# Optimization experiments

Measured on AMD Instinct MI355X. Metric: run time of the kernel, lower is better.

Reference implementation:

```python
import jax, jax.numpy as jnp
import numpy as np

R = 32          # grid_resolution
C_DIM = 128
HID = 128
N_BLOCKS = 5
PAD = 0.1
N_FREQ = 10

def setup_inputs() -> dict:
    key = jax.random.key(0)
    ks = jax.random.split(key, 10)
    B, T = 4, 65536
    s = 0.05
    return {
        "p": jax.random.uniform(ks[0], (B, T, 3), jnp.float32, -0.5, 0.5),
        "fc_pos_w": jax.random.normal(ks[1], (60, 2 * HID), jnp.float32) * s,
        "fc_pos_b": jax.random.normal(ks[2], (2 * HID,), jnp.float32) * s,
        "fc0_w": jax.random.normal(ks[3], (N_BLOCKS, 2 * HID, HID), jnp.float32) * s,
        "fc0_b": jax.random.normal(ks[4], (N_BLOCKS, HID), jnp.float32) * s,
        "fc1_w": jax.random.normal(ks[5], (N_BLOCKS, HID, HID), jnp.float32) * s,
        "fc1_b": jax.random.normal(ks[6], (N_BLOCKS, HID), jnp.float32) * s,
        "sc_w": jax.random.normal(ks[7], (N_BLOCKS, 2 * HID, HID), jnp.float32) * s,
        "fc_c_w": jax.random.normal(ks[8], (HID, C_DIM), jnp.float32) * s,
        "fc_c_b": jax.random.normal(ks[9], (C_DIM,), jnp.float32) * s,
    }

def _pos_enc(p):
    # NeRF-style: per frequency append sin then cos -> [B,T,3*2*10]=60
    freqs = (2.0 ** jnp.arange(N_FREQ, dtype=p.dtype)) * np.pi
    outs = []
    for i in range(N_FREQ):
        outs.append(jnp.sin(freqs[i] * p))
        outs.append(jnp.cos(freqs[i] * p))
    return jnp.concatenate(outs, axis=-1)

def _grid_index(p):
    # normalize_3d_coordinate + coordinate2index (3d)
    p_nor = p / (1.0 + PAD + 1e-3) + 0.5
    p_nor = jnp.clip(p_nor, 0.0, 1.0 - 1e-3)
    xi = (p_nor * R).astype(jnp.int32)
    return xi[..., 0] + R * (xi[..., 1] + R * xi[..., 2])  # [B,T]

def _resblock(x, w0, b0, w1, b1, ws):
    # ResnetBlockFC: fc_0(relu(x)) -> fc_1(relu(net)); shortcut Linear(no bias)
    net = jnp.maximum(x, 0) @ w0 + b0
    dx = jnp.maximum(net, 0) @ w1 + b1
    return x @ ws + dx

def _seg_max(c, idx):  # c [T,D], idx [T]
    return jax.ops.segment_max(c, idx, num_segments=R ** 3)

def _seg_sum(c, idx):
    return jax.ops.segment_sum(c, idx, num_segments=R ** 3)

def reference(p, fc_pos_w, fc_pos_b, fc0_w, fc0_b, fc1_w, fc1_b, sc_w, fc_c_w, fc_c_b):
    B = p.shape[0]
    index = _grid_index(p)                               # [B,T] int32
    net = _pos_enc(p) @ fc_pos_w + fc_pos_b              # [B,T,256]
    net = _resblock(net, fc0_w[0], fc0_b[0], fc1_w[0], fc1_b[0], sc_w[0])  # [B,T,128]
    for i in range(1, N_BLOCKS):
        # pool_local: scatter_max per voxel, gather back at each point
        fea = jax.vmap(_seg_max)(net, index)             # [B,R^3,128]
        pooled = jnp.take_along_axis(fea, index[..., None], axis=1)  # [B,T,128]
        net = jnp.concatenate([net, pooled], axis=-1)    # [B,T,256]
        net = _resblock(net, fc0_w[i], fc0_b[i], fc1_w[i], fc1_b[i], sc_w[i])
    c = net @ fc_c_w + fc_c_b                            # [B,T,128]
    # generate_grid_features: scatter_mean into R^3 voxels (empty voxels -> 0)
    sums = jax.vmap(_seg_sum)(c, index)                  # [B,R^3,128]
    cnt = jax.vmap(_seg_sum)(jnp.ones(index.shape + (1,), c.dtype), index)
    mean = sums / jnp.maximum(cnt, 1.0)
    fea_grid = mean.transpose(0, 2, 1).reshape(B, C_DIM, R, R, R)
    return fea_grid
```

## Files before the change

### kernel.cpp

```cpp
#include <hip/hip_runtime.h>

typedef _Float16 hf;
typedef _Float16 hf8 __attribute__((ext_vector_type(8)));
typedef float f32x4 __attribute__((ext_vector_type(4)));

static constexpr int BATCH = 4;
static constexpr int TPTS  = 65536;
static constexpr int NPTS  = BATCH * TPTS;
static constexpr int R3    = 32768;
static constexpr int NVOX  = BATCH * R3;

static constexpr int OFF_WPOS = 0;
static constexpr int OFF_W0   = 16384;
static constexpr int OFF_W1   = 180224;
static constexpr int OFF_WSC  = 262144;
static constexpr int OFF_WC   = 425984;
static constexpr int NCHUNKS  = 55296;

__device__ constexpr int kpat(int g, int j) { return (j & 3) + 4 * g + 16 * (j >> 2); }

#define MFMA16(a, b, c) __builtin_amdgcn_mfma_f32_16x16x32_f16((a), (b), (c), 0, 0, 0)

__device__ inline hf8 relu8(hf8 a) {
#pragma unroll
  for (int i = 0; i < 8; ++i) a[i] = (a[i] > (hf)0) ? a[i] : (hf)0;
  return a;
}
__device__ inline f32x4 splat4(float v) {
  f32x4 r; r[0] = v; r[1] = v; r[2] = v; r[3] = v; return r;
}
__device__ inline hf8 ldfrag(const hf* __restrict__ base, int kc, int nt, int NT, int lane) {
  return *(const hf8*)(base + (((size_t)(kc * NT + nt) * 64 + lane) << 3));
}

__global__ __launch_bounds__(256) void k_prep(
    const float* __restrict__ wpos, const float* __restrict__ w0,
    const float* __restrict__ w1,  const float* __restrict__ wsc,
    const float* __restrict__ wc,  hf* __restrict__ fr)
{
  const int cid = blockIdx.x * 256 + threadIdx.x;
  if (cid >= NCHUNKS) return;
  const float* src; hf* dst; int NT, N, kmax, loc;
  if (cid < 2048) {
    src = wpos; dst = fr + OFF_WPOS; NT = 16; N = 256; kmax = 60; loc = cid;
  } else if (cid < 22528) {
    int l5 = cid - 2048; int i = l5 >> 12; loc = l5 & 4095;
    src = w0 + (size_t)i * 32768; dst = fr + OFF_W0 + (size_t)i * 32768;
    NT = 8; N = 128; kmax = 256;
  } else if (cid < 32768) {
    int l5 = cid - 22528; int i = l5 >> 11; loc = l5 & 2047;
    src = w1 + (size_t)i * 16384; dst = fr + OFF_W1 + (size_t)i * 16384;
    NT = 8; N = 128; kmax = 128;
  } else if (cid < 53248) {
    int l5 = cid - 32768; int i = l5 >> 12; loc = l5 & 4095;
    src = wsc + (size_t)i * 32768; dst = fr + OFF_WSC + (size_t)i * 32768;
    NT = 8; N = 128; kmax = 256;
  } else {
    loc = cid - 53248; src = wc; dst = fr + OFF_WC; NT = 8; N = 128; kmax = 128;
  }
  const int lane = loc & 63;
  const int rest = loc >> 6;
  const int nt = rest % NT, kc = rest / NT;
  const int g = lane >> 4;
  const int n = nt * 16 + (lane & 15);
  union { hf8 h; hf f[8]; } o;
#pragma unroll
  for (int j = 0; j < 8; ++j) {
    int k = kc * 32 + kpat(g, j);
    o.f[j] = (k < kmax) ? (hf)src[(size_t)k * N + n] : (hf)0;
  }
  *(hf8*)(dst + ((size_t)loc << 3)) = o.h;
}

__global__ __launch_bounds__(256) void k_idxcnt(
    const float* __restrict__ p, int* __restrict__ idxbuf, int* __restrict__ cnt)
{
  const int t = blockIdx.x * 256 + threadIdx.x;
  const float px = p[(size_t)t * 3 + 0];
  const float py = p[(size_t)t * 3 + 1];
  const float pz = p[(size_t)t * 3 + 2];
  float nx = fminf(fmaxf(px / 1.101f + 0.5f, 0.0f), 0.999f);
  float ny = fminf(fmaxf(py / 1.101f + 0.5f, 0.0f), 0.999f);
  float nz = fminf(fmaxf(pz / 1.101f + 0.5f, 0.0f), 0.999f);
  const int iv = (int)(nx * 32.f) + 32 * (int)(ny * 32.f) + 1024 * (int)(nz * 32.f);
  idxbuf[t] = iv;
  atomicAdd(&cnt[((t >> 16) << 15) | iv], 1);
}

__global__ __launch_bounds__(256) void k_scan(
    const int* __restrict__ cnt, int* __restrict__ start, int* __restrict__ total)
{
  __shared__ int s[256];
  __shared__ int base_s;
  const int tid = threadIdx.x;
  const int v0 = blockIdx.x * 512;
  const int a = cnt[v0 + 2 * tid], b = cnt[v0 + 2 * tid + 1];
  const int sum = a + b;
  s[tid] = sum;
  __syncthreads();
  for (int off = 1; off < 256; off <<= 1) {
    int x = (tid >= off) ? s[tid - off] : 0;
    __syncthreads();
    s[tid] += x;
    __syncthreads();
  }
  if (tid == 255) base_s = atomicAdd(total, s[255]);
  __syncthreads();
  const int excl = base_s + s[tid] - sum;
  start[v0 + 2 * tid]     = excl;
  start[v0 + 2 * tid + 1] = excl + a;
}

__global__ __launch_bounds__(256) void k_fill(
    int* __restrict__ idxbuf, int* __restrict__ start, int* __restrict__ svox)
{
  const int t = blockIdx.x * 256 + threadIdx.x;
  const int bv = ((t >> 16) << 15) | idxbuf[t];
  const int pos = atomicAdd(&start[bv], 1);
  svox[pos] = bv;
  idxbuf[t] = pos;
}

__global__ __launch_bounds__(256, 4) void k_fused0(
    const float* __restrict__ p, const hf* __restrict__ fr,
    const float* __restrict__ bpos,
    const hf* __restrict__ w0f, const hf* __restrict__ w1f,
    const hf* __restrict__ wscf,
    const float* __restrict__ b0, const float* __restrict__ b1,
    const int* __restrict__ spos, hf* __restrict__ net)
{
  __shared__ __align__(16) hf swX[16384];
  __shared__ int sp[64];
  const int tid = threadIdx.x;
  const int wv = tid >> 6, lane = tid & 63;
  const int r = lane & 15, g = lane >> 4;
  const int t0 = blockIdx.x * 64;

  if (tid < 64) sp[tid] = spos[t0 + tid];

  if (tid < 64) {
    const int mt = tid >> 4, rr = tid & 15;
    *(unsigned long long*)(swX + (((mt * 2 + 1) * 64 + 48 + rr) << 3) + 4) = 0ull;
  }
#pragma unroll
  for (int i = 0; i < 8; ++i) {
    const int tau = tid + i * 256;
    if (tau >= 1920) break;
    const int pt = (int)(((unsigned)tau * 34953u) >> 20);
    const int a  = tau - pt * 30;
    const int fi = (a * 11) >> 5;
    const int comp = a - 3 * fi;
    const float pc = p[(size_t)(t0 + pt) * 3 + comp];
    const float ang = (float)(1 << fi) * 3.14159274101257324f * pc;
    const float sv = __sinf(ang), cv = __cosf(ang);
    const int mt = pt >> 4, rr = pt & 15;
    const int ks = 6 * fi + comp;
    {
      const int kc = ks >> 5, kk = ks & 31, gg = (kk >> 2) & 3;
      const int e = (kk & 3) + 4 * (kk >> 4);
      swX[(((mt * 2 + kc) * 64 + gg * 16 + rr) << 3) + e] = (hf)sv;
    }
    {
      const int kco = ks + 3;
      const int kc = kco >> 5, kk = kco & 31, gg = (kk >> 2) & 3;
      const int e = (kk & 3) + 4 * (kk >> 4);
      swX[(((mt * 2 + kc) * 64 + gg * 16 + rr) << 3) + e] = (hf)cv;
    }
  }
  __syncthreads();

  f32x4 acc[4][4];
#pragma unroll
  for (int nf = 0; nf < 4; ++nf) {
    float bv = bpos[wv * 64 + nf * 16 + r];
#pragma unroll
    for (int mf = 0; mf < 4; ++mf) acc[mf][nf] = splat4(bv);
  }
#pragma unroll
  for (int kc = 0; kc < 2; ++kc) {
    hf8 a[4];
#pragma unroll
    for (int mf = 0; mf < 4; ++mf)
      a[mf] = *(const hf8*)(swX + (((mf * 2 + kc) * 64 + lane) << 3));
#pragma unroll
    for (int nf = 0; nf < 4; ++nf) {
      hf8 b = ldfrag(fr + OFF_WPOS, kc, wv * 4 + nf, 16, lane);
#pragma unroll
      for (int mf = 0; mf < 4; ++mf) acc[mf][nf] = MFMA16(a[mf], b, acc[mf][nf]);
    }
  }
  __syncthreads();

#pragma unroll
  for (int mf = 0; mf < 4; ++mf)
#pragma unroll
    for (int nf = 0; nf < 4; ++nf)
#pragma unroll
      for (int reg = 0; reg < 4; ++reg) {
        int rr = 4 * g + reg;
        int c  = wv * 64 + nf * 16 + r;
        int kc = c >> 5;
        int kk = c & 31;
        int gg = (kk >> 2) & 3;
        int e  = (kk & 3) + 4 * (kk >> 4);
        int slot = gg * 16 + ((rr + gg) & 15);
        swX[(((size_t)(mf * 8 + kc) * 64 + slot) << 3) + e] = (hf)acc[mf][nf][reg];
      }
  __syncthreads();

  const int wm = wv >> 1, wn = wv & 1;
  const int lidx = g * 16 + ((r + g) & 15);

  f32x4 h[2][4], d[2][4];
#pragma unroll
  for (int nf = 0; nf < 4; ++nf) {
    const int n = wn * 64 + nf * 16 + r;
    const float bh = b0[n], bd = b1[n];
#pragma unroll
    for (int mf = 0; mf < 2; ++mf) { h[mf][nf] = splat4(bh); d[mf][nf] = splat4(bd); }
  }
#pragma unroll 2
  for (int kc = 0; kc < 8; ++kc) {
    hf8 a[2], ar[2];
#pragma unroll
    for (int mf = 0; mf < 2; ++mf) {
      a[mf] = *(const hf8*)(swX + (((size_t)((wm * 2 + mf) * 8 + kc) * 64 + lidx) << 3));
      ar[mf] = relu8(a[mf]);
    }
#pragma unroll
    for (int nf = 0; nf < 4; ++nf) {
      hf8 bw0 = ldfrag(w0f, kc, wn * 4 + nf, 8, lane);
      hf8 bws = ldfrag(wscf, kc, wn * 4 + nf, 8, lane);
#pragma unroll
      for (int mf = 0; mf < 2; ++mf) {
        h[mf][nf] = MFMA16(ar[mf], bw0, h[mf][nf]);
        d[mf][nf] = MFMA16(a[mf],  bws, d[mf][nf]);
      }
    }
  }
  __syncthreads();

#pragma unroll
  for (int mf = 0; mf < 2; ++mf)
#pragma unroll
    for (int nf = 0; nf < 4; ++nf)
#pragma unroll
      for (int reg = 0; reg < 4; ++reg) {
        int m = wm * 32 + mf * 16 + 4 * g + reg;
        int k = wn * 64 + nf * 16 + r;
        float hv = fmaxf(h[mf][nf][reg], 0.f);
        int mt = m >> 4, rr = m & 15;
        int kc = k >> 5, kk = k & 31;
        int gg = (kk >> 2) & 3;
        int e = (kk & 3) + 4 * (kk >> 4);
        int slot = gg * 16 + ((rr + gg) & 15);
        swX[(((size_t)(mt * 4 + kc) * 64 + slot) << 3) + e] = (hf)hv;
      }
  __syncthreads();

#pragma unroll
  for (int kc = 0; kc < 4; ++kc) {
    hf8 a[2];
#pragma unroll
    for (int mf = 0; mf < 2; ++mf)
      a[mf] = *(const hf8*)(swX + (((size_t)((wm * 2 + mf) * 4 + kc) * 64 + lidx) << 3));
#pragma unroll
    for (int nf = 0; nf < 4; ++nf) {
      hf8 bw1 = ldfrag(w1f, kc, wn * 4 + nf, 8, lane);
#pragma unroll
      for (int mf = 0; mf < 2; ++mf) d[mf][nf] = MFMA16(a[mf], bw1, d[mf][nf]);
    }
  }

#pragma unroll
  for (int mf = 0; mf < 2; ++mf)
#pragma unroll
    for (int nf = 0; nf < 4; ++nf)
#pragma unroll
      for (int reg = 0; reg < 4; ++reg) {
        int m = wm * 32 + mf * 16 + 4 * g + reg;
        int n = wn * 64 + nf * 16 + r;
        net[(size_t)sp[m] * 128 + n] = (hf)d[mf][nf][reg];
      }
}

__global__ __launch_bounds__(256) void k_pool(
    const hf* __restrict__ net, const int* __restrict__ start,
    const int* __restrict__ cnt, hf* __restrict__ fea)
{
  const int gid = blockIdx.x * 256 + threadIdx.x;
  const int bv = gid >> 4;
  const int q = gid & 15;
  const int n = cnt[bv];
  if (n == 0) return;
  const int end = start[bv], beg = end - n;
  float m[8];
#pragma unroll
  for (int e = 0; e < 8; ++e) m[e] = -1e30f;
  for (int i = beg; i < end; ++i) {
    union { uint4 u; hf h[8]; } x;
    x.u = *(const uint4*)(net + (size_t)i * 128 + 8 * q);
#pragma unroll
    for (int e = 0; e < 8; ++e) m[e] = fmaxf(m[e], (float)x.h[e]);
  }
  union { uint4 u; hf h[8]; } o;
#pragma unroll
  for (int e = 0; e < 8; ++e) o.h[e] = (hf)m[e];
  *(uint4*)(fea + ((size_t)bv << 7) + 8 * q) = o.u;
}

__global__ __launch_bounds__(256, 2) void k_res(
    hf* __restrict__ net, const hf* __restrict__ fea,
    const int* __restrict__ svox,
    const hf* __restrict__ w0f, const hf* __restrict__ w1f,
    const hf* __restrict__ wscf,
    const float* __restrict__ b0, const float* __restrict__ b1)
{
  __shared__ __align__(16) hf swX[32768];
  const int tid = threadIdx.x;
  const int wv = tid >> 6, lane = tid & 63;
  const int r = lane & 15, g = lane >> 4;
  const int wm = wv >> 1, wn = wv & 1;
  const int t0 = blockIdx.x * 128;
  const int lidx = g * 16 + ((r + g) & 15);

  for (int cc = tid; cc < 4096; cc += 256) {
    const int cl = cc & 63;
    const int kc = (cc >> 6) & 7;
    const int mt = cc >> 9;
    const int rr = cl & 15, gg = cl >> 4;
    const int t = t0 + mt * 16 + rr;
    const int c1 = kc * 32 + 4 * gg;
    union { hf8 h; uint2 u2[2]; } x;
    const hf* srcp;
    if (kc < 4) {
      srcp = net + (size_t)t * 128 + c1;
    } else {
      srcp = fea + (((size_t)svox[t]) << 7) + (c1 - 128);
    }
    x.u2[0] = *(const uint2*)(srcp);
    x.u2[1] = *(const uint2*)(srcp + 16);
    const int slot = gg * 16 + ((rr + gg) & 15);
    *(hf8*)(swX + (((size_t)((cc & ~63) + slot)) << 3)) = x.h;
  }
  __syncthreads();

  f32x4 h[4][4], d[4][4];
#pragma unroll
  for (int nf = 0; nf < 4; ++nf) {
    const int n = wn * 64 + nf * 16 + r;
    const float bh = b0[n], bd = b1[n];
#pragma unroll
    for (int mf = 0; mf < 4; ++mf) { h[mf][nf] = splat4(bh); d[mf][nf] = splat4(bd); }
  }
#pragma unroll 2
  for (int kc = 0; kc < 8; ++kc) {
    hf8 a[4], ar[4];
#pragma unroll
    for (int mf = 0; mf < 4; ++mf) {
      a[mf] = *(const hf8*)(swX + (((size_t)((wm * 4 + mf) * 8 + kc) * 64 + lidx) << 3));
      ar[mf] = relu8(a[mf]);
    }
#pragma unroll
    for (int nf = 0; nf < 4; ++nf) {
      hf8 bw0 = ldfrag(w0f, kc, wn * 4 + nf, 8, lane);
      hf8 bws = ldfrag(wscf, kc, wn * 4 + nf, 8, lane);
#pragma unroll
      for (int mf = 0; mf < 4; ++mf) {
        h[mf][nf] = MFMA16(ar[mf], bw0, h[mf][nf]);
        d[mf][nf] = MFMA16(a[mf],  bws, d[mf][nf]);
      }
    }
  }
  __syncthreads();

#pragma unroll
  for (int mf = 0; mf < 4; ++mf)
#pragma unroll
    for (int nf = 0; nf < 4; ++nf)
#pragma unroll
      for (int reg = 0; reg < 4; ++reg) {
        int m = wm * 64 + mf * 16 + 4 * g + reg;
        int k = wn * 64 + nf * 16 + r;
        float hv = fmaxf(h[mf][nf][reg], 0.f);
        int mt = m >> 4, rr = m & 15;
        int kc = k >> 5, kk = k & 31;
        int gg = (kk >> 2) & 3;
        int e = (kk & 3) + 4 * (kk >> 4);
        int slot = gg * 16 + ((rr + gg) & 15);
        swX[(((size_t)(mt * 4 + kc) * 64 + slot) << 3) + e] = (hf)hv;
      }
  __syncthreads();

#pragma unroll
  for (int kc = 0; kc < 4; ++kc) {
    hf8 a[4];
#pragma unroll
    for (int mf = 0; mf < 4; ++mf)
      a[mf] = *(const hf8*)(swX + (((size_t)((wm * 4 + mf) * 4 + kc) * 64 + lidx) << 3));
#pragma unroll
    for (int nf = 0; nf < 4; ++nf) {
      hf8 bw1 = ldfrag(w1f, kc, wn * 4 + nf, 8, lane);
#pragma unroll
      for (int mf = 0; mf < 4; ++mf) d[mf][nf] = MFMA16(a[mf], bw1, d[mf][nf]);
    }
  }

#pragma unroll
  for (int mf = 0; mf < 4; ++mf)
#pragma unroll
    for (int nf = 0; nf < 4; ++nf)
#pragma unroll
      for (int reg = 0; reg < 4; ++reg) {
        int m = wm * 64 + mf * 16 + 4 * g + reg;
        int n = wn * 64 + nf * 16 + r;
        net[(size_t)(t0 + m) * 128 + n] = (hf)d[mf][nf][reg];
      }
}

__global__ __launch_bounds__(256, 4) void k_fcc(
    hf* __restrict__ net, const hf* __restrict__ wcf, const float* __restrict__ bc)
{
  __shared__ __align__(16) hf swX[16384];
  const int tid = threadIdx.x;
  const int wv = tid >> 6, lane = tid & 63;
  const int r = lane & 15, g = lane >> 4;
  const int wm = wv >> 1, wn = wv & 1;
  const int t0 = blockIdx.x * 128;

  for (int cc = tid; cc < 2048; cc += 256) {
    const int cl = cc & 63;
    const int kc = (cc >> 6) & 3;
    const int mt = cc >> 8;
    const int rr = cl & 15, gg = cl >> 4;
    const int t = t0 + mt * 16 + rr;
    const int c1 = kc * 32 + 4 * gg;
    union { hf8 h; uint2 u2[2]; } x;
    const hf* srcp = net + (size_t)t * 128 + c1;
    x.u2[0] = *(const uint2*)(srcp);
    x.u2[1] = *(const uint2*)(srcp + 16);
    *(hf8*)(swX + ((size_t)cc << 3)) = x.h;
  }
  __syncthreads();

  f32x4 d[4][4];
#pragma unroll
  for (int nf = 0; nf < 4; ++nf) {
    float bv = bc[wn * 64 + nf * 16 + r];
#pragma unroll
    for (int mf = 0; mf < 4; ++mf) d[mf][nf] = splat4(bv);
  }
#pragma unroll
  for (int kc = 0; kc < 4; ++kc) {
    hf8 a[4];
#pragma unroll
    for (int mf = 0; mf < 4; ++mf)
      a[mf] = *(const hf8*)(swX + (((size_t)((wm * 4 + mf) * 4 + kc) * 64 + lane) << 3));
#pragma unroll
    for (int nf = 0; nf < 4; ++nf) {
      hf8 b = ldfrag(wcf, kc, wn * 4 + nf, 8, lane);
#pragma unroll
      for (int mf = 0; mf < 4; ++mf) d[mf][nf] = MFMA16(a[mf], b, d[mf][nf]);
    }
  }

#pragma unroll
  for (int mf = 0; mf < 4; ++mf)
#pragma unroll
    for (int nf = 0; nf < 4; ++nf)
#pragma unroll
      for (int reg = 0; reg < 4; ++reg) {
        int m = wm * 64 + mf * 16 + 4 * g + reg;
        int n = wn * 64 + nf * 16 + r;
        net[(size_t)(t0 + m) * 128 + n] = (hf)d[mf][nf][reg];
      }
}

__global__ __launch_bounds__(256) void k_write(
    const hf* __restrict__ cbuf, const int* __restrict__ start,
    const int* __restrict__ cnt, float* __restrict__ out)
{
  __shared__ float tile[128 * 65];
  const int tid = threadIdx.x;
  const int grp = tid >> 4, q = tid & 15;
  const int g0 = blockIdx.x * 64;
  for (int vl = grp; vl < 64; vl += 16) {
    const int bv = g0 + vl;
    const int n = cnt[bv];
    const int end = start[bv], beg = end - n;
    float s[8] = {0, 0, 0, 0, 0, 0, 0, 0};
    for (int i = beg; i < end; ++i) {
      union { uint4 u; hf h[8]; } x;
      x.u = *(const uint4*)(cbuf + (size_t)i * 128 + 8 * q);
#pragma unroll
      for (int e = 0; e < 8; ++e) s[e] += (float)x.h[e];
    }
    const float inv = 1.0f / fmaxf((float)n, 1.0f);
#pragma unroll
    for (int e = 0; e < 8; ++e) tile[(8 * q + e) * 65 + vl] = s[e] * inv;
  }
  __syncthreads();
  const int b = g0 >> 15, v0 = g0 & 32767;
  for (int i = tid; i < 8192; i += 256) {
    const int c = i >> 6, vl = i & 63;
    out[(((size_t)(b * 128 + c)) << 15) + v0 + vl] = tile[c * 65 + vl];
  }
}

extern "C" void kernel_launch(void* const* d_in, const int* in_sizes, int n_in,
                              void* d_out, int out_size, void* d_ws, size_t ws_size,
                              hipStream_t stream)
{
  const float* p    = (const float*)d_in[0];
  const float* wpos = (const float*)d_in[1];
  const float* bpos = (const float*)d_in[2];
  const float* w0   = (const float*)d_in[3];
  const float* b0   = (const float*)d_in[4];
  const float* w1   = (const float*)d_in[5];
  const float* b1   = (const float*)d_in[6];
  const float* wsc  = (const float*)d_in[7];
  const float* wc   = (const float*)d_in[8];
  const float* bc   = (const float*)d_in[9];

  char* ws = (char*)d_ws;
  int* idxbuf = (int*)ws;
  hf*  net    = (hf*)(ws + (1u << 20));
  hf*  fea    = (hf*)(ws + (65u << 20));
  int* cnt32  = (int*)(ws + (97u << 20));
  int* total  = (int*)(ws + (97u << 20) + 0x80000);
  int* startb = (int*)(ws + (97u << 20) + 0x80400);
  int* svox   = (int*)(ws + (97u << 20) + 0x100400);
  hf*  fr     = (hf*)d_out;

  k_prep<<<216, 256, 0, stream>>>(wpos, w0, w1, wsc, wc, fr);

  hipMemsetAsync(cnt32, 0, 0x80000 + 0x400, stream);
  k_idxcnt<<<NPTS / 256, 256, 0, stream>>>(p, idxbuf, cnt32);
  k_scan<<<NVOX / 512, 256, 0, stream>>>(cnt32, startb, total);
  k_fill<<<NPTS / 256, 256, 0, stream>>>(idxbuf, startb, svox);

  k_fused0<<<NPTS / 64, 256, 0, stream>>>(p, fr, bpos,
      fr + OFF_W0, fr + OFF_W1, fr + OFF_WSC, b0, b1, idxbuf, net);

  for (int i = 1; i < 5; ++i) {
    k_pool<<<(NVOX * 16) / 256, 256, 0, stream>>>(net, startb, cnt32, fea);
    k_res<<<NPTS / 128, 256, 0, stream>>>(net, fea, svox,
        fr + OFF_W0 + (size_t)i * 32768, fr + OFF_W1 + (size_t)i * 16384,
        fr + OFF_WSC + (size_t)i * 32768, b0 + i * 128, b1 + i * 128);
  }

  k_fcc<<<NPTS / 128, 256, 0, stream>>>(net, fr + OFF_WC, bc);
  k_write<<<NVOX / 64, 256, 0, stream>>>(net, startb, cnt32, (float*)d_out);
}
```

Measured before the change: 636.1 us.

## Fuse final fc_c projection into last resblock and pool by sorted point runs

The final fc_c GEMM is folded into the last k_res launch. The block output is staged back into LDS in the swizzled A-fragment layout and multiplied by the fc_c weights, so one global write and read of net is avoided. k_pool now walks sorted points (svox) in runs of equal voxel id instead of launching 16 threads per voxel, including empty ones. This removes the idle threads for empty voxels, but load balance now depends on run length, and a run that crosses a group boundary is scanned entirely by the group where it starts.

```diff
diff --git a/kernel.cpp b/kernel.cpp
--- a/kernel.cpp
+++ b/kernel.cpp
@@ -285,36 +285,44 @@
 }
 
 __global__ __launch_bounds__(256) void k_pool(
-    const hf* __restrict__ net, const int* __restrict__ start,
-    const int* __restrict__ cnt, hf* __restrict__ fea)
-{
-  const int gid = blockIdx.x * 256 + threadIdx.x;
-  const int bv = gid >> 4;
-  const int q = gid & 15;
-  const int n = cnt[bv];
-  if (n == 0) return;
-  const int end = start[bv], beg = end - n;
-  float m[8];
-#pragma unroll
-  for (int e = 0; e < 8; ++e) m[e] = -1e30f;
-  for (int i = beg; i < end; ++i) {
-    union { uint4 u; hf h[8]; } x;
-    x.u = *(const uint4*)(net + (size_t)i * 128 + 8 * q);
-#pragma unroll
-    for (int e = 0; e < 8; ++e) m[e] = fmaxf(m[e], (float)x.h[e]);
-  }
-  union { uint4 u; hf h[8]; } o;
-#pragma unroll
-  for (int e = 0; e < 8; ++e) o.h[e] = (hf)m[e];
-  *(uint4*)(fea + ((size_t)bv << 7) + 8 * q) = o.u;
-}
-
+    const hf* __restrict__ net, const int* __restrict__ svox,
+    hf* __restrict__ fea)
+{
+  const int tid = threadIdx.x;
+  const int grp = tid >> 4, q = tid & 15;
+  const int gbeg = blockIdx.x * 128 + grp * 8;
+  const int gend = gbeg + 8;
+  int i = gbeg;
+  while (i < gend) {
+    const int v = svox[i];
+    if (i != 0 && svox[i - 1] == v) { ++i; continue; }
+    float m[8];
+#pragma unroll
+    for (int e = 0; e < 8; ++e) m[e] = -1e30f;
+    int j = i;
+    do {
+      union { uint4 u; hf h[8]; } x;
+      x.u = *(const uint4*)(net + (size_t)j * 128 + 8 * q);
+#pragma unroll
+      for (int e = 0; e < 8; ++e) m[e] = fmaxf(m[e], (float)x.h[e]);
+      ++j;
+    } while (j < NPTS && svox[j] == v);
+    union { uint4 u; hf h[8]; } o;
+#pragma unroll
+    for (int e = 0; e < 8; ++e) o.h[e] = (hf)m[e];
+    *(uint4*)(fea + ((size_t)v << 7) + 8 * q) = o.u;
+    i = j;
+  }
+}
+
+template <int LAST>
 __global__ __launch_bounds__(256, 2) void k_res(
     hf* __restrict__ net, const hf* __restrict__ fea,
     const int* __restrict__ svox,
     const hf* __restrict__ w0f, const hf* __restrict__ w1f,
     const hf* __restrict__ wscf,
-    const float* __restrict__ b0, const float* __restrict__ b1)
+    const float* __restrict__ b0, const float* __restrict__ b1,
+    const hf* __restrict__ wcf, const float* __restrict__ bc)
 {
   __shared__ __align__(16) hf swX[32768];
   const int tid = threadIdx.x;
@@ -406,74 +414,67 @@
     }
   }
 
-#pragma unroll
-  for (int mf = 0; mf < 4; ++mf)
-#pragma unroll
-    for (int nf = 0; nf < 4; ++nf)
-#pragma unroll
-      for (int reg = 0; reg < 4; ++reg) {
-        int m = wm * 64 + mf * 16 + 4 * g + reg;
-        int n = wn * 64 + nf * 16 + r;
-        net[(size_t)(t0 + m) * 128 + n] = (hf)d[mf][nf][reg];
-      }
-}
-
-__global__ __launch_bounds__(256, 4) void k_fcc(
-    hf* __restrict__ net, const hf* __restrict__ wcf, const float* __restrict__ bc)
-{
-  __shared__ __align__(16) hf swX[16384];
-  const int tid = threadIdx.x;
-  const int wv = tid >> 6, lane = tid & 63;
-  const int r = lane & 15, g = lane >> 4;
-  const int wm = wv >> 1, wn = wv & 1;
-  const int t0 = blockIdx.x * 128;
-
-  for (int cc = tid; cc < 2048; cc += 256) {
-    const int cl = cc & 63;
-    const int kc = (cc >> 6) & 3;
-    const int mt = cc >> 8;
-    const int rr = cl & 15, gg = cl >> 4;
-    const int t = t0 + mt * 16 + rr;
-    const int c1 = kc * 32 + 4 * gg;
-    union { hf8 h; uint2 u2[2]; } x;
-    const hf* srcp = net + (size_t)t * 128 + c1;
-    x.u2[0] = *(const uint2*)(srcp);
-    x.u2[1] = *(const uint2*)(srcp + 16);
-    *(hf8*)(swX + ((size_t)cc << 3)) = x.h;
-  }
-  __syncthreads();
-
-  f32x4 d[4][4];
-#pragma unroll
-  for (int nf = 0; nf < 4; ++nf) {
-    float bv = bc[wn * 64 + nf * 16 + r];
-#pragma unroll
-    for (int mf = 0; mf < 4; ++mf) d[mf][nf] = splat4(bv);
-  }
-#pragma unroll
-  for (int kc = 0; kc < 4; ++kc) {
-    hf8 a[4];
+  if (LAST) {
+    __syncthreads();
 #pragma unroll
     for (int mf = 0; mf < 4; ++mf)
-      a[mf] = *(const hf8*)(swX + (((size_t)((wm * 4 + mf) * 4 + kc) * 64 + lane) << 3));
+#pragma unroll
+      for (int nf = 0; nf < 4; ++nf)
+#pragma unroll
+        for (int reg = 0; reg < 4; ++reg) {
+          int m = wm * 64 + mf * 16 + 4 * g + reg;
+          int k = wn * 64 + nf * 16 + r;
+          int mt = m >> 4, rr = m & 15;
+          int kc = k >> 5, kk = k & 31;
+          int gg = (kk >> 2) & 3;
+          int e = (kk & 3) + 4 * (kk >> 4);
+          int slot = gg * 16 + ((rr + gg) & 15);
+          swX[(((size_t)(mt * 4 + kc) * 64 + slot) << 3) + e] = (hf)d[mf][nf][reg];
+        }
+    __syncthreads();
+
+    f32x4 c2[4][4];
 #pragma unroll
     for (int nf = 0; nf < 4; ++nf) {
-      hf8 b = ldfrag(wcf, kc, wn * 4 + nf, 8, lane);
-#pragma unroll
-      for (int mf = 0; mf < 4; ++mf) d[mf][nf] = MFMA16(a[mf], b, d[mf][nf]);
-    }
-  }
-
-#pragma unroll
-  for (int mf = 0; mf < 4; ++mf)
-#pragma unroll
-    for (int nf = 0; nf < 4; ++nf)
-#pragma unroll
-      for (int reg = 0; reg < 4; ++reg) {
-        int m = wm * 64 + mf * 16 + 4 * g + reg;
-        int n = wn * 64 + nf * 16 + r;
-        net[(size_t)(t0 + m) * 128 + n] = (hf)d[mf][nf][reg];
-      }
+      float bv = bc[wn * 64 + nf * 16 + r];
+#pragma unroll
+      for (int mf = 0; mf < 4; ++mf) c2[mf][nf] = splat4(bv);
+    }
+#pragma unroll
+    for (int kc = 0; kc < 4; ++kc) {
+      hf8 a[4];
+#pragma unroll
+      for (int mf = 0; mf < 4; ++mf)
+        a[mf] = *(const hf8*)(swX + (((size_t)((wm * 4 + mf) * 4 + kc) * 64 + lidx) << 3));
+#pragma unroll
+      for (int nf = 0; nf < 4; ++nf) {
+        hf8 bw = ldfrag(wcf, kc, wn * 4 + nf, 8, lane);
+#pragma unroll
+        for (int mf = 0; mf < 4; ++mf) c2[mf][nf] = MFMA16(a[mf], bw, c2[mf][nf]);
+      }
+    }
+#pragma unroll
+    for (int mf = 0; mf < 4; ++mf)
+#pragma unroll
+      for (int nf = 0; nf < 4; ++nf)
+#pragma unroll
+        for (int reg = 0; reg < 4; ++reg) {
+          int m = wm * 64 + mf * 16 + 4 * g + reg;
+          int n = wn * 64 + nf * 16 + r;
+          net[(size_t)(t0 + m) * 128 + n] = (hf)c2[mf][nf][reg];
+        }
+  } else {
+#pragma unroll
+    for (int mf = 0; mf < 4; ++mf)
+#pragma unroll
+      for (int nf = 0; nf < 4; ++nf)
+#pragma unroll
+        for (int reg = 0; reg < 4; ++reg) {
+          int m = wm * 64 + mf * 16 + 4 * g + reg;
+          int n = wn * 64 + nf * 16 + r;
+          net[(size_t)(t0 + m) * 128 + n] = (hf)d[mf][nf][reg];
+        }
+  }
 }
 
 __global__ __launch_bounds__(256) void k_write(
@@ -542,13 +543,18 @@
   k_fused0<<<NPTS / 64, 256, 0, stream>>>(p, fr, bpos,
       fr + OFF_W0, fr + OFF_W1, fr + OFF_WSC, b0, b1, idxbuf, net);
 
-  for (int i = 1; i < 5; ++i) {
-    k_pool<<<(NVOX * 16) / 256, 256, 0, stream>>>(net, startb, cnt32, fea);
-    k_res<<<NPTS / 128, 256, 0, stream>>>(net, fea, svox,
+  for (int i = 1; i < 4; ++i) {
+    k_pool<<<NPTS / 128, 256, 0, stream>>>(net, svox, fea);
+    k_res<0><<<NPTS / 128, 256, 0, stream>>>(net, fea, svox,
         fr + OFF_W0 + (size_t)i * 32768, fr + OFF_W1 + (size_t)i * 16384,
-        fr + OFF_WSC + (size_t)i * 32768, b0 + i * 128, b1 + i * 128);
-  }
-
-  k_fcc<<<NPTS / 128, 256, 0, stream>>>(net, fr + OFF_WC, bc);
+        fr + OFF_WSC + (size_t)i * 32768, b0 + i * 128, b1 + i * 128,
+        nullptr, nullptr);
+  }
+  k_pool<<<NPTS / 128, 256, 0, stream>>>(net, svox, fea);
+  k_res<1><<<NPTS / 128, 256, 0, stream>>>(net, fea, svox,
+      fr + OFF_W0 + (size_t)4 * 32768, fr + OFF_W1 + (size_t)4 * 16384,
+      fr + OFF_WSC + (size_t)4 * 32768, b0 + 4 * 128, b1 + 4 * 128,
+      fr + OFF_WC, bc);
+
   k_write<<<NVOX / 64, 256, 0, stream>>>(net, startb, cnt32, (float*)d_out);
 }
```

New measurement: 619.2 us. 2.7% less time.
